# Kernel optimization log

Measured on AMD Instinct MI355X. Metric: run time of the kernel, lower is better.

Reference implementation:

```python
import jax, jax.numpy as jnp
import numpy as np

B, IN, U = 4096, 256, 128
G, LW, LB = 1000, 64, 32


def setup_inputs() -> dict:
    key = jax.random.key(0)
    ks = jax.random.split(key, 9)
    return {
        "x": jax.random.normal(ks[0], (B, IN), dtype=jnp.float32),
        "eps_w": jax.random.normal(ks[1], (B, LW), dtype=jnp.float32),
        "eps_b": jax.random.normal(ks[2], (B, LB), dtype=jnp.float32),
        "zw_mu": jax.random.normal(ks[3], (G, LW), dtype=jnp.float32) * 0.05,
        "zw_sigma": jax.random.normal(ks[4], (G, LW), dtype=jnp.float32),
        "Wf": jax.random.normal(ks[5], (LW, IN * U), dtype=jnp.float32) * (1.0 / np.sqrt(LW)),
        "zb_mu": jnp.zeros((G, LB), dtype=jnp.float32),
        "zb_sigma": jax.random.normal(ks[6], (G, LB), dtype=jnp.float32),
        "Bf": jax.random.normal(ks[7], (LB, U), dtype=jnp.float32) * (1.0 / np.sqrt(LB)),
        "gid": jax.random.randint(ks[8], (B,), 0, G, dtype=jnp.int32),
    }


def reference(x, eps_w, eps_b, zw_mu, zw_sigma, Wf, zb_mu, zb_sigma, Bf, gid):
    # --- multilevel weights: gather group posterior, reparameterized sample ---
    mu_w = zw_mu[gid]                                  # [B, LW]
    sig_w = jax.nn.softplus(zw_sigma[gid])             # [B, LW]
    zw_samp = mu_w + sig_w * eps_w                     # [B, LW]
    w = (zw_samp @ Wf).reshape(B, IN, U)               # factor out to per-example weights
    # --- multilevel bias ---
    mu_b = zb_mu[gid]                                  # [B, LB]
    sig_b = jax.nn.softplus(zb_sigma[gid])             # [B, LB]
    b = (mu_b + sig_b * eps_b) @ Bf                    # [B, U]
    # --- batched per-example matmul: w^T @ x  (tf.matmul(w, x, transpose_a=True)) ---
    out = jnp.einsum("bi,biu->bu", x, w) + b           # [B, U]
    return out  # activation is None (linear)
```

## Files before the change

kernel.cpp:

```cpp
#include <hip/hip_runtime.h>
#include <hip/hip_bf16.h>
#include <stdint.h>

#define B_SZ   4096
#define IN_SZ  256
#define U_SZ   128
#define G_SZ   1000
#define LW_SZ  64
#define LB_SZ  32
#define K_SZ   (LW_SZ * IN_SZ)

#define BM     128
#define BK     64
#define KSPL   16
#define NSTEP  16
#define NTILE  (K_SZ / BK)
#define CHUNK  (BK * U_SZ)

typedef __attribute__((ext_vector_type(8))) short  bf16x8;
typedef __attribute__((ext_vector_type(4))) float  f32x4;
typedef __attribute__((ext_vector_type(8))) _Float16 f16x8;
typedef __attribute__((ext_vector_type(2))) _Float16 f16x2;
typedef __attribute__((ext_vector_type(4))) _Float16 f16x4;

typedef const void __attribute__((address_space(1)))* gas_ptr;
typedef void __attribute__((address_space(3)))* las_ptr;

__device__ __forceinline__ ushort f2bf(float f) {
    unsigned u = __float_as_uint(f);
    u += 0x7fffu + ((u >> 16) & 1u);
    return (ushort)(u >> 16);
}

__device__ __forceinline__ float softplus_f(float v) {
    return fmaxf(v, 0.0f) + log1pf(__expf(-fabsf(v)));
}

__global__ __launch_bounds__(256) void fmd_prep(
    const float* __restrict__ Wf, const float* __restrict__ x,
    short* __restrict__ wfT, short* __restrict__ xh)
{
    const int tid = threadIdx.x;
    if (blockIdx.x < NTILE) {
        const int t = blockIdx.x;
        __shared__ float lds[64 * 133];
        #pragma unroll
        for (int it = 0; it < 8; ++it) {
            int idx = it * 256 + tid;
            int kk = idx >> 5, u4 = idx & 31;
            float4 v = *reinterpret_cast<const float4*>(&Wf[(t * 64 + kk) * U_SZ + u4 * 4]);
            *reinterpret_cast<float4*>(&lds[kk * 133 + u4 * 4]) = v;
        }
        __syncthreads();
        short* chunk = wfT + t * CHUNK;
        #pragma unroll
        for (int g = 0; g < 4; ++g) {
            int p = g * 2048 + tid * 8;
            int u = p >> 6;
            int cc = p & 63;
            int kk0 = cc ^ ((u & 7) << 3);
            union { _Float16 h[8]; f16x8 v; } pk;
            #pragma unroll
            for (int j = 0; j < 8; ++j)
                pk.h[j] = (_Float16)lds[(kk0 + j) * 133 + u];
            *reinterpret_cast<f16x8*>(&chunk[p]) = pk.v;
        }
    } else {
        const int bb = blockIdx.x - NTILE;
        const int mt = bb >> 2, c = bb & 3;
        short* chunk = xh + bb * CHUNK;
        #pragma unroll
        for (int g = 0; g < 4; ++g) {
            int p = g * 2048 + tid * 8;
            int r = p >> 6;
            int cc0 = (p & 63) ^ ((r & 7) << 3);
            const float* src = &x[(mt * BM + r) * IN_SZ + c * 64 + cc0];
            float4 a = *reinterpret_cast<const float4*>(src);
            float4 b = *reinterpret_cast<const float4*>(src + 4);
            union { _Float16 h[8]; f16x8 v; } pk;
            pk.h[0] = (_Float16)a.x; pk.h[1] = (_Float16)a.y;
            pk.h[2] = (_Float16)a.z; pk.h[3] = (_Float16)a.w;
            pk.h[4] = (_Float16)b.x; pk.h[5] = (_Float16)b.y;
            pk.h[6] = (_Float16)b.z; pk.h[7] = (_Float16)b.w;
            *reinterpret_cast<f16x8*>(&chunk[p]) = pk.v;
        }
    }
}

__global__ __launch_bounds__(256, 2) void fmd_gemm5(
    const short* __restrict__ xh,
    const short* __restrict__ wfT,
    const float* __restrict__ zw_mu,
    const float* __restrict__ zw_sigma,
    const float* __restrict__ eps_w,
    const int*   __restrict__ gid,
    _Float16*    __restrict__ part)
{
    const int tid  = threadIdx.x;
    const int lane = tid & 63;
    const int wid  = tid >> 6;
    const int wr   = wid >> 1;
    const int wc   = wid & 1;
    const int bid  = blockIdx.x;
    const int ks   = bid & (KSPL - 1);
    const int mt   = bid >> 4;
    const int m0   = mt * BM;

    __shared__ short As[CHUNK];
    __shared__ short Bs[3][CHUNK];

    f16x2 zwp[4][4];
    #pragma unroll
    for (int m = 0; m < 4; ++m) {
        int row = wr * 64 + m * 16 + (lane & 15);
        int b   = m0 + row;
        int g   = gid[b];
        float4 mu = *reinterpret_cast<const float4*>(&zw_mu[g * LW_SZ + ks * 4]);
        float4 sg = *reinterpret_cast<const float4*>(&zw_sigma[g * LW_SZ + ks * 4]);
        float4 ep = *reinterpret_cast<const float4*>(&eps_w[b * LW_SZ + ks * 4]);
        float v0 = mu.x + softplus_f(sg.x) * ep.x;
        float v1 = mu.y + softplus_f(sg.y) * ep.y;
        float v2 = mu.z + softplus_f(sg.z) * ep.z;
        float v3 = mu.w + softplus_f(sg.w) * ep.w;
        _Float16 h0 = (_Float16)v0, h1 = (_Float16)v1, h2 = (_Float16)v2, h3 = (_Float16)v3;
        zwp[m][0] = (f16x2){h0, h0};
        zwp[m][1] = (f16x2){h1, h1};
        zwp[m][2] = (f16x2){h2, h2};
        zwp[m][3] = (f16x2){h3, h3};
    }

    const int soff = wid * 2048 + lane * 8;
    const int doff = wid * 2048;

    {
        const short* sB0 = wfT + (ks * 16 + 0) * CHUNK;
        const short* sA0 = xh + (mt * 4 + 0) * CHUNK;
        const short* sB1 = wfT + (ks * 16 + 4) * CHUNK;
        #pragma unroll
        for (int j = 0; j < 4; ++j)
            __builtin_amdgcn_global_load_lds((gas_ptr)(sB0 + soff + j * 512),
                                             (las_ptr)(&Bs[0][doff + j * 512]), 16, 0, 0);
        #pragma unroll
        for (int j = 0; j < 4; ++j)
            __builtin_amdgcn_global_load_lds((gas_ptr)(sA0 + soff + j * 512),
                                             (las_ptr)(&As[doff + j * 512]), 16, 0, 0);
        #pragma unroll
        for (int j = 0; j < 4; ++j)
            __builtin_amdgcn_global_load_lds((gas_ptr)(sB1 + soff + j * 512),
                                             (las_ptr)(&Bs[1][doff + j * 512]), 16, 0, 0);
    }
    asm volatile("s_waitcnt vmcnt(4)" ::: "memory");
    __builtin_amdgcn_s_barrier();

    f32x4 acc[4][4];
    #pragma unroll
    for (int m = 0; m < 4; ++m)
        #pragma unroll
        for (int n = 0; n < 4; ++n)
            acc[m][n] = (f32x4){0.f, 0.f, 0.f, 0.f};

    for (int c = 0; c < 4; ++c) {
        union { f16x8 v8; f16x2 v2[4]; } areg[2][4];

        #pragma unroll
        for (int li = 0; li < 4; ++li) {
            const int s = c * 4 + li;

            if (s + 2 < NSTEP) {
                const int s2 = s + 2;
                const short* sB = wfT + (ks * 16 + (s2 & 3) * 4 + (s2 >> 2)) * CHUNK;
                short* dB = &Bs[s2 % 3][doff];
                #pragma unroll
                for (int j = 0; j < 4; ++j)
                    __builtin_amdgcn_global_load_lds((gas_ptr)(sB + soff + j * 512),
                                                     (las_ptr)(dB + j * 512), 16, 0, 0);
            }
            if (li == 1 && c < 3) {
                const short* sA = xh + (mt * 4 + c + 1) * CHUNK;
                #pragma unroll
                for (int j = 0; j < 4; ++j)
                    __builtin_amdgcn_global_load_lds((gas_ptr)(sA + soff + j * 512),
                                                     (las_ptr)(&As[doff + j * 512]), 16, 0, 0);
            }
            __builtin_amdgcn_sched_barrier(0);

            if (li == 0) {
                #pragma unroll
                for (int kb = 0; kb < 2; ++kb)
                    #pragma unroll
                    for (int m = 0; m < 4; ++m) {
                        int row = wr * 64 + m * 16 + (lane & 15);
                        int si = (row * BK + kb * 32 + (lane >> 4) * 8) ^ ((row & 7) << 3);
                        areg[kb][m].v8 = *reinterpret_cast<const f16x8*>(&As[si]);
                    }
            }

            const short* Bb = Bs[s % 3];
            __builtin_amdgcn_s_setprio(1);
            #pragma unroll
            for (int kb = 0; kb < 2; ++kb) {
                union { f16x8 v8; f16x2 v2[4]; } bfv[4], as_[4];
                #pragma unroll
                for (int n = 0; n < 4; ++n) {
                    int rowu = wc * 64 + n * 16 + (lane & 15);
                    int si = (rowu * BK + kb * 32 + (lane >> 4) * 8) ^ ((rowu & 7) << 3);
                    bfv[n].v8 = *reinterpret_cast<const f16x8*>(&Bb[si]);
                }
                #pragma unroll
                for (int m = 0; m < 4; ++m) {
                    #pragma unroll
                    for (int w = 0; w < 4; ++w)
                        as_[m].v2[w] = areg[kb][m].v2[w] * zwp[m][li];
                }
                #pragma unroll
                for (int m = 0; m < 4; ++m)
                    #pragma unroll
                    for (int n = 0; n < 4; ++n)
                        acc[m][n] = __builtin_amdgcn_mfma_f32_16x16x32_f16(
                            as_[m].v8, bfv[n].v8, acc[m][n], 0, 0, 0);
            }
            __builtin_amdgcn_s_setprio(0);

            if (li == 0) {
                asm volatile("s_waitcnt vmcnt(4) lgkmcnt(0)" ::: "memory");
                __builtin_amdgcn_s_barrier();
            } else if (li == 1) {
                if (c < 3) { asm volatile("s_waitcnt vmcnt(8) lgkmcnt(0)" ::: "memory"); }
                else       { asm volatile("s_waitcnt vmcnt(4) lgkmcnt(0)" ::: "memory"); }
                __builtin_amdgcn_s_barrier();
            } else if (li == 2) {
                if (c < 3) { asm volatile("s_waitcnt vmcnt(8) lgkmcnt(0)" ::: "memory"); }
                else       { asm volatile("s_waitcnt vmcnt(0) lgkmcnt(0)" ::: "memory"); }
                __builtin_amdgcn_s_barrier();
            } else {
                if (s != NSTEP - 1) {
                    asm volatile("s_waitcnt vmcnt(4) lgkmcnt(0)" ::: "memory");
                    __builtin_amdgcn_s_barrier();
                }
            }
        }
    }

    _Float16* dst = part + (size_t)ks * (B_SZ * U_SZ);
    #pragma unroll
    for (int m = 0; m < 4; ++m) {
        int row0 = m0 + wr * 64 + m * 16 + ((lane >> 4) << 2);
        #pragma unroll
        for (int n = 0; n < 4; ++n) {
            int col = wc * 64 + n * 16 + (lane & 15);
            #pragma unroll
            for (int j = 0; j < 4; ++j)
                __builtin_nontemporal_store((_Float16)acc[m][n][j],
                                            &dst[(row0 + j) * U_SZ + col]);
        }
    }
}

__global__ __launch_bounds__(256) void fmd_reduce3(
    const _Float16* __restrict__ part,
    const float* __restrict__ eps_b,
    const float* __restrict__ zb_mu,
    const float* __restrict__ zb_sigma,
    const float* __restrict__ Bf,
    const int*   __restrict__ gid,
    float*       __restrict__ out)
{
    const int tid = threadIdx.x;
    const int bid = blockIdx.x;
    const int i8  = bid * 256 + tid;
    const int r   = tid >> 4;
    const int u0  = (tid & 15) * 8;

    __shared__ float zb[16][33];
    {
        int e = tid;
        int rr = e >> 5, cc = e & 31;
        int b2 = bid * 16 + rr;
        int g  = gid[b2];
        zb[rr][cc] = zb_mu[g * LB_SZ + cc]
                   + softplus_f(zb_sigma[g * LB_SZ + cc]) * eps_b[b2 * LB_SZ + cc];
        e += 256; rr = e >> 5; cc = e & 31;
        b2 = bid * 16 + rr;
        g  = gid[b2];
        zb[rr][cc] = zb_mu[g * LB_SZ + cc]
                   + softplus_f(zb_sigma[g * LB_SZ + cc]) * eps_b[b2 * LB_SZ + cc];
    }
    __syncthreads();

    f32x4 a0 = (f32x4){0.f, 0.f, 0.f, 0.f};
    f32x4 a1 = (f32x4){0.f, 0.f, 0.f, 0.f};
    #pragma unroll
    for (int l = 0; l < LB_SZ; ++l) {
        float z = zb[r][l];
        f32x4 b0 = *reinterpret_cast<const f32x4*>(&Bf[l * U_SZ + u0]);
        f32x4 b1 = *reinterpret_cast<const f32x4*>(&Bf[l * U_SZ + u0 + 4]);
        a0 += z * b0;
        a1 += z * b1;
    }

    #pragma unroll
    for (int ks = 0; ks < KSPL; ++ks) {
        f16x8 p = __builtin_nontemporal_load(
            reinterpret_cast<const f16x8*>(&part[(size_t)ks * (B_SZ * U_SZ) + (size_t)i8 * 8]));
        a0[0] += (float)p[0]; a0[1] += (float)p[1];
        a0[2] += (float)p[2]; a0[3] += (float)p[3];
        a1[0] += (float)p[4]; a1[1] += (float)p[5];
        a1[2] += (float)p[6]; a1[3] += (float)p[7];
    }
    *reinterpret_cast<f32x4*>(&out[(size_t)i8 * 8])     = a0;
    *reinterpret_cast<f32x4*>(&out[(size_t)i8 * 8 + 4]) = a1;
}

__global__ __launch_bounds__(256) void fmd_bias(
    const float* __restrict__ eps_b,
    const float* __restrict__ zb_mu,
    const float* __restrict__ zb_sigma,
    const float* __restrict__ Bf,
    const int*   __restrict__ gid,
    float*       __restrict__ out)
{
    const int half = threadIdx.x >> 7;
    const int u    = threadIdx.x & 127;
    const int b    = blockIdx.x * 2 + half;

    __shared__ float zb[2][LB_SZ];
    if (u < LB_SZ) {
        int g = gid[b];
        float sg = softplus_f(zb_sigma[g * LB_SZ + u]);
        zb[half][u] = zb_mu[g * LB_SZ + u] + sg * eps_b[b * LB_SZ + u];
    }
    __syncthreads();

    float acc = 0.0f;
    #pragma unroll
    for (int l = 0; l < LB_SZ; ++l)
        acc += zb[half][l] * Bf[l * U_SZ + u];
    out[b * U_SZ + u] = acc;
}

__global__ __launch_bounds__(256, 2) void fmd_gemm_legacy(
    const float* __restrict__ x,
    const float* __restrict__ eps_w,
    const float* __restrict__ zw_mu,
    const float* __restrict__ zw_sigma,
    const float* __restrict__ Wf,
    const int*   __restrict__ gid,
    float*       __restrict__ out)
{
    const int tid  = threadIdx.x;
    const int lane = tid & 63;
    const int wid  = tid >> 6;
    const int wr   = wid >> 1;
    const int wc   = wid & 1;
    const int bid  = blockIdx.x;
    const int ks   = bid & (KSPL - 1);
    const int mt   = bid >> 4;
    const int m0   = mt * BM;

    __shared__ short As[BM * BK];
    __shared__ short Bs[U_SZ * BK];
    __shared__ float zw_s[BM][4];

    for (int it = tid; it < BM * 4; it += 256) {
        int r = it >> 2, lloc = it & 3;
        int b = m0 + r;
        int g = gid[b];
        int l = ks * 4 + lloc;
        float sg = softplus_f(zw_sigma[g * LW_SZ + l]);
        zw_s[r][lloc] = zw_mu[g * LW_SZ + l] + sg * eps_w[b * LW_SZ + l];
    }

    f32x4 acc[4][4];
    #pragma unroll
    for (int m = 0; m < 4; ++m)
        #pragma unroll
        for (int n = 0; n < 4; ++n)
            acc[m][n] = (f32x4){0.f, 0.f, 0.f, 0.f};

    for (int s = 0; s < NSTEP; ++s) {
        __syncthreads();
        const int li = s >> 2;
        const int i0 = (s & 3) * BK;
        const int k0 = ks * (K_SZ / KSPL) + s * BK;

        #pragma unroll
        for (int it = 0; it < 8; ++it) {
            int idx = it * 256 + tid;
            int r = idx >> 4, c4 = idx & 15;
            float4 xv = *reinterpret_cast<const float4*>(&x[(m0 + r) * IN_SZ + i0 + c4 * 4]);
            float zw = zw_s[r][li];
            ushort h0 = f2bf(xv.x * zw), h1 = f2bf(xv.y * zw);
            ushort h2 = f2bf(xv.z * zw), h3 = f2bf(xv.w * zw);
            unsigned long long pw = (unsigned long long)h0
                                  | ((unsigned long long)h1 << 16)
                                  | ((unsigned long long)h2 << 32)
                                  | ((unsigned long long)h3 << 48);
            int si = (r * BK + c4 * 4) ^ ((r & 7) << 3);
            *reinterpret_cast<unsigned long long*>(&As[si]) = pw;
        }
        #pragma unroll
        for (int it = 0; it < 4; ++it) {
            int idx = it * 256 + tid;
            int u = idx & 127, kg = idx >> 7;
            union { ushort h[8]; bf16x8 v; } pk;
            #pragma unroll
            for (int j = 0; j < 8; ++j)
                pk.h[j] = f2bf(Wf[(k0 + kg * 8 + j) * U_SZ + u]);
            int si = (u * BK + kg * 8) ^ ((u & 7) << 3);
            *reinterpret_cast<bf16x8*>(&Bs[si]) = pk.v;
        }
        __syncthreads();

        #pragma unroll
        for (int kb = 0; kb < 2; ++kb) {
            bf16x8 af[4], bfr[4];
            #pragma unroll
            for (int m = 0; m < 4; ++m) {
                int row = wr * 64 + m * 16 + (lane & 15);
                int si = (row * BK + kb * 32 + (lane >> 4) * 8) ^ ((row & 7) << 3);
                af[m] = *reinterpret_cast<const bf16x8*>(&As[si]);
            }
            #pragma unroll
            for (int n = 0; n < 4; ++n) {
                int rowu = wc * 64 + n * 16 + (lane & 15);
                int si = (rowu * BK + kb * 32 + (lane >> 4) * 8) ^ ((rowu & 7) << 3);
                bfr[n] = *reinterpret_cast<const bf16x8*>(&Bs[si]);
            }
            #pragma unroll
            for (int m = 0; m < 4; ++m)
                #pragma unroll
                for (int n = 0; n < 4; ++n)
                    acc[m][n] = __builtin_amdgcn_mfma_f32_16x16x32_bf16(af[m], bfr[n], acc[m][n], 0, 0, 0);
        }
    }

    #pragma unroll
    for (int m = 0; m < 4; ++m) {
        int row0 = m0 + wr * 64 + m * 16 + ((lane >> 4) << 2);
        #pragma unroll
        for (int n = 0; n < 4; ++n) {
            int col = wc * 64 + n * 16 + (lane & 15);
            #pragma unroll
            for (int j = 0; j < 4; ++j)
                atomicAdd(&out[(row0 + j) * U_SZ + col], acc[m][n][j]);
        }
    }
}

extern "C" void kernel_launch(void* const* d_in, const int* in_sizes, int n_in,
                              void* d_out, int out_size, void* d_ws, size_t ws_size,
                              hipStream_t stream) {
    const float* x        = (const float*)d_in[0];
    const float* eps_w    = (const float*)d_in[1];
    const float* eps_b    = (const float*)d_in[2];
    const float* zw_mu    = (const float*)d_in[3];
    const float* zw_sigma = (const float*)d_in[4];
    const float* Wf       = (const float*)d_in[5];
    const float* zb_mu    = (const float*)d_in[6];
    const float* zb_sigma = (const float*)d_in[7];
    const float* Bf       = (const float*)d_in[8];
    const int*   gid      = (const int*)d_in[9];
    float* out = (float*)d_out;

    const size_t WFT_BYTES  = (size_t)K_SZ * U_SZ * 2;
    const size_t XH_OFF     = WFT_BYTES;
    const size_t XH_BYTES   = (size_t)B_SZ * IN_SZ * 2;
    const size_t PART_OFF   = XH_OFF + XH_BYTES;
    const size_t PART_BYTES = (size_t)KSPL * B_SZ * U_SZ * 2;

    if (ws_size >= PART_OFF + PART_BYTES) {
        short*     wfT  = (short*)d_ws;
        short*     xh   = (short*)((char*)d_ws + XH_OFF);
        _Float16*  part = (_Float16*)((char*)d_ws + PART_OFF);
        fmd_prep<<<NTILE + (B_SZ / BM) * 4, 256, 0, stream>>>(Wf, x, wfT, xh);
        fmd_gemm5<<<(B_SZ / BM) * KSPL, 256, 0, stream>>>(
            xh, wfT, zw_mu, zw_sigma, eps_w, gid, part);
        fmd_reduce3<<<(B_SZ * U_SZ) / 2048, 256, 0, stream>>>(
            part, eps_b, zb_mu, zb_sigma, Bf, gid, out);
    } else {
        fmd_bias<<<B_SZ / 2, 256, 0, stream>>>(eps_b, zb_mu, zb_sigma, Bf, gid, out);
        fmd_gemm_legacy<<<(B_SZ / BM) * KSPL, 256, 0, stream>>>(
            x, eps_w, zw_mu, zw_sigma, Wf, gid, out);
    }
}
```

Measured before the change: 48.84 us.

## Pre-swizzle operands into MFMA fragment order and load directly to registers

```diff
diff --git a/kernel.cpp b/kernel.cpp
--- a/kernel.cpp
+++ b/kernel.cpp
@@ -11,20 +11,15 @@
 #define K_SZ   (LW_SZ * IN_SZ)
 
 #define BM     128
-#define BK     64
 #define KSPL   16
 #define NSTEP  16
-#define NTILE  (K_SZ / BK)
-#define CHUNK  (BK * U_SZ)
+#define NTILE  (K_SZ / 64)
+#define TSH    8192
 
 typedef __attribute__((ext_vector_type(8))) short  bf16x8;
 typedef __attribute__((ext_vector_type(4))) float  f32x4;
 typedef __attribute__((ext_vector_type(8))) _Float16 f16x8;
 typedef __attribute__((ext_vector_type(2))) _Float16 f16x2;
-typedef __attribute__((ext_vector_type(4))) _Float16 f16x4;
-
-typedef const void __attribute__((address_space(1)))* gas_ptr;
-typedef void __attribute__((address_space(3)))* las_ptr;
 
 __device__ __forceinline__ ushort f2bf(float f) {
     unsigned u = __float_as_uint(f);
@@ -34,6 +29,14 @@
 
 __device__ __forceinline__ float softplus_f(float v) {
     return fmaxf(v, 0.0f) + log1pf(__expf(-fabsf(v)));
+}
+
+__device__ __forceinline__ f16x8 mulzw(f16x8 a, f16x2 z) {
+    union { f16x8 v8; f16x2 v2[4]; } in, out;
+    in.v8 = a;
+    #pragma unroll
+    for (int w = 0; w < 4; ++w) out.v2[w] = in.v2[w] * z;
+    return out.v8;
 }
 
 __global__ __launch_bounds__(256) void fmd_prep(
@@ -52,29 +55,36 @@
             *reinterpret_cast<float4*>(&lds[kk * 133 + u4 * 4]) = v;
         }
         __syncthreads();
-        short* chunk = wfT + t * CHUNK;
-        #pragma unroll
-        for (int g = 0; g < 4; ++g) {
-            int p = g * 2048 + tid * 8;
-            int u = p >> 6;
-            int cc = p & 63;
-            int kk0 = cc ^ ((u & 7) << 3);
+        short* tile = wfT + t * TSH;
+        #pragma unroll
+        for (int it = 0; it < 4; ++it) {
+            int p = it * 256 + tid;
+            int kb  = p >> 9;
+            int u16 = (p >> 6) & 7;
+            int l   = p & 63;
+            int u   = u16 * 16 + (l & 15);
+            int kk0 = kb * 32 + (l >> 4) * 8;
             union { _Float16 h[8]; f16x8 v; } pk;
             #pragma unroll
             for (int j = 0; j < 8; ++j)
                 pk.h[j] = (_Float16)lds[(kk0 + j) * 133 + u];
-            *reinterpret_cast<f16x8*>(&chunk[p]) = pk.v;
+            *reinterpret_cast<f16x8*>(&tile[p * 8]) = pk.v;
         }
     } else {
         const int bb = blockIdx.x - NTILE;
         const int mt = bb >> 2, c = bb & 3;
-        short* chunk = xh + bb * CHUNK;
-        #pragma unroll
-        for (int g = 0; g < 4; ++g) {
-            int p = g * 2048 + tid * 8;
-            int r = p >> 6;
-            int cc0 = (p & 63) ^ ((r & 7) << 3);
-            const float* src = &x[(mt * BM + r) * IN_SZ + c * 64 + cc0];
+        short* tile = xh + bb * TSH;
+        #pragma unroll
+        for (int it = 0; it < 4; ++it) {
+            int p = it * 256 + tid;
+            int frag = p >> 6;
+            int l    = p & 63;
+            int wr2  = frag >> 3;
+            int m2   = (frag >> 1) & 3;
+            int kb   = frag & 1;
+            int row  = mt * 128 + wr2 * 64 + m2 * 16 + (l & 15);
+            int col  = c * 64 + kb * 32 + (l >> 4) * 8;
+            const float* src = &x[row * IN_SZ + col];
             float4 a = *reinterpret_cast<const float4*>(src);
             float4 b = *reinterpret_cast<const float4*>(src + 4);
             union { _Float16 h[8]; f16x8 v; } pk;
@@ -82,12 +92,12 @@
             pk.h[2] = (_Float16)a.z; pk.h[3] = (_Float16)a.w;
             pk.h[4] = (_Float16)b.x; pk.h[5] = (_Float16)b.y;
             pk.h[6] = (_Float16)b.z; pk.h[7] = (_Float16)b.w;
-            *reinterpret_cast<f16x8*>(&chunk[p]) = pk.v;
-        }
-    }
-}
-
-__global__ __launch_bounds__(256, 2) void fmd_gemm5(
+            *reinterpret_cast<f16x8*>(&tile[p * 8]) = pk.v;
+        }
+    }
+}
+
+__global__ __launch_bounds__(256, 2) void fmd_gemm6(
     const short* __restrict__ xh,
     const short* __restrict__ wfT,
     const float* __restrict__ zw_mu,
@@ -105,9 +115,7 @@
     const int ks   = bid & (KSPL - 1);
     const int mt   = bid >> 4;
     const int m0   = mt * BM;
-
-    __shared__ short As[CHUNK];
-    __shared__ short Bs[3][CHUNK];
+    const int lane8 = lane * 8;
 
     f16x2 zwp[4][4];
     #pragma unroll
@@ -129,28 +137,26 @@
         zwp[m][3] = (f16x2){h3, h3};
     }
 
-    const int soff = wid * 2048 + lane * 8;
-    const int doff = wid * 2048;
+    f16x8 areg[2][2][4];
+    f16x8 breg[2][2][4];
 
     {
-        const short* sB0 = wfT + (ks * 16 + 0) * CHUNK;
-        const short* sA0 = xh + (mt * 4 + 0) * CHUNK;
-        const short* sB1 = wfT + (ks * 16 + 4) * CHUNK;
-        #pragma unroll
-        for (int j = 0; j < 4; ++j)
-            __builtin_amdgcn_global_load_lds((gas_ptr)(sB0 + soff + j * 512),
-                                             (las_ptr)(&Bs[0][doff + j * 512]), 16, 0, 0);
-        #pragma unroll
-        for (int j = 0; j < 4; ++j)
-            __builtin_amdgcn_global_load_lds((gas_ptr)(sA0 + soff + j * 512),
-                                             (las_ptr)(&As[doff + j * 512]), 16, 0, 0);
-        #pragma unroll
-        for (int j = 0; j < 4; ++j)
-            __builtin_amdgcn_global_load_lds((gas_ptr)(sB1 + soff + j * 512),
-                                             (las_ptr)(&Bs[1][doff + j * 512]), 16, 0, 0);
-    }
-    asm volatile("s_waitcnt vmcnt(4)" ::: "memory");
-    __builtin_amdgcn_s_barrier();
+        const short* ap = xh + (mt * 4 + 0) * TSH;
+        #pragma unroll
+        for (int kb = 0; kb < 2; ++kb)
+            #pragma unroll
+            for (int m = 0; m < 4; ++m)
+                areg[0][kb][m] = *reinterpret_cast<const f16x8*>(
+                    &ap[((wr * 4 + m) * 2 + kb) * 512 + lane8]);
+        const int t0 = (ks * 4 + 0) * 4 + 0;
+        const short* bp = wfT + t0 * TSH;
+        #pragma unroll
+        for (int kb = 0; kb < 2; ++kb)
+            #pragma unroll
+            for (int n = 0; n < 4; ++n)
+                breg[0][kb][n] = *reinterpret_cast<const f16x8*>(
+                    &bp[(kb * 8 + wc * 4 + n) * 512 + lane8]);
+    }
 
     f32x4 acc[4][4];
     #pragma unroll
@@ -159,84 +165,45 @@
         for (int n = 0; n < 4; ++n)
             acc[m][n] = (f32x4){0.f, 0.f, 0.f, 0.f};
 
+    #pragma unroll
     for (int c = 0; c < 4; ++c) {
-        union { f16x8 v8; f16x2 v2[4]; } areg[2][4];
-
         #pragma unroll
         for (int li = 0; li < 4; ++li) {
             const int s = c * 4 + li;
 
-            if (s + 2 < NSTEP) {
-                const int s2 = s + 2;
-                const short* sB = wfT + (ks * 16 + (s2 & 3) * 4 + (s2 >> 2)) * CHUNK;
-                short* dB = &Bs[s2 % 3][doff];
-                #pragma unroll
-                for (int j = 0; j < 4; ++j)
-                    __builtin_amdgcn_global_load_lds((gas_ptr)(sB + soff + j * 512),
-                                                     (las_ptr)(dB + j * 512), 16, 0, 0);
-            }
-            if (li == 1 && c < 3) {
-                const short* sA = xh + (mt * 4 + c + 1) * CHUNK;
-                #pragma unroll
-                for (int j = 0; j < 4; ++j)
-                    __builtin_amdgcn_global_load_lds((gas_ptr)(sA + soff + j * 512),
-                                                     (las_ptr)(&As[doff + j * 512]), 16, 0, 0);
-            }
-            __builtin_amdgcn_sched_barrier(0);
-
-            if (li == 0) {
+            if (s + 1 < NSTEP) {
+                const int sn = s + 1;
+                const int t  = (ks * 4 + (sn & 3)) * 4 + (sn >> 2);
+                const short* bp = wfT + t * TSH;
                 #pragma unroll
                 for (int kb = 0; kb < 2; ++kb)
                     #pragma unroll
-                    for (int m = 0; m < 4; ++m) {
-                        int row = wr * 64 + m * 16 + (lane & 15);
-                        int si = (row * BK + kb * 32 + (lane >> 4) * 8) ^ ((row & 7) << 3);
-                        areg[kb][m].v8 = *reinterpret_cast<const f16x8*>(&As[si]);
-                    }
+                    for (int n = 0; n < 4; ++n)
+                        breg[sn & 1][kb][n] = *reinterpret_cast<const f16x8*>(
+                            &bp[(kb * 8 + wc * 4 + n) * 512 + lane8]);
             }
-
-            const short* Bb = Bs[s % 3];
-            __builtin_amdgcn_s_setprio(1);
+            if (li == 2 && c < 3) {
+                const short* ap = xh + (mt * 4 + c + 1) * TSH;
+                #pragma unroll
+                for (int kb = 0; kb < 2; ++kb)
+                    #pragma unroll
+                    for (int m = 0; m < 4; ++m)
+                        areg[(c + 1) & 1][kb][m] = *reinterpret_cast<const f16x8*>(
+                            &ap[((wr * 4 + m) * 2 + kb) * 512 + lane8]);
+            }
+
             #pragma unroll
             for (int kb = 0; kb < 2; ++kb) {
-                union { f16x8 v8; f16x2 v2[4]; } bfv[4], as_[4];
+                f16x8 as_[4];
                 #pragma unroll
-                for (int n = 0; n < 4; ++n) {
-                    int rowu = wc * 64 + n * 16 + (lane & 15);
-                    int si = (rowu * BK + kb * 32 + (lane >> 4) * 8) ^ ((rowu & 7) << 3);
-                    bfv[n].v8 = *reinterpret_cast<const f16x8*>(&Bb[si]);
-                }
-                #pragma unroll
-                for (int m = 0; m < 4; ++m) {
-                    #pragma unroll
-                    for (int w = 0; w < 4; ++w)
-                        as_[m].v2[w] = areg[kb][m].v2[w] * zwp[m][li];
-                }
+                for (int m = 0; m < 4; ++m)
+                    as_[m] = mulzw(areg[c & 1][kb][m], zwp[m][li]);
                 #pragma unroll
                 for (int m = 0; m < 4; ++m)
                     #pragma unroll
                     for (int n = 0; n < 4; ++n)
                         acc[m][n] = __builtin_amdgcn_mfma_f32_16x16x32_f16(
-                            as_[m].v8, bfv[n].v8, acc[m][n], 0, 0, 0);
-            }
-            __builtin_amdgcn_s_setprio(0);
-
-            if (li == 0) {
-                asm volatile("s_waitcnt vmcnt(4) lgkmcnt(0)" ::: "memory");
-                __builtin_amdgcn_s_barrier();
-            } else if (li == 1) {
-                if (c < 3) { asm volatile("s_waitcnt vmcnt(8) lgkmcnt(0)" ::: "memory"); }
-                else       { asm volatile("s_waitcnt vmcnt(4) lgkmcnt(0)" ::: "memory"); }
-                __builtin_amdgcn_s_barrier();
-            } else if (li == 2) {
-                if (c < 3) { asm volatile("s_waitcnt vmcnt(8) lgkmcnt(0)" ::: "memory"); }
-                else       { asm volatile("s_waitcnt vmcnt(0) lgkmcnt(0)" ::: "memory"); }
-                __builtin_amdgcn_s_barrier();
-            } else {
-                if (s != NSTEP - 1) {
-                    asm volatile("s_waitcnt vmcnt(4) lgkmcnt(0)" ::: "memory");
-                    __builtin_amdgcn_s_barrier();
-                }
+                            as_[m], breg[s & 1][kb][n], acc[m][n], 0, 0, 0);
             }
         }
     }
@@ -250,13 +217,12 @@
             int col = wc * 64 + n * 16 + (lane & 15);
             #pragma unroll
             for (int j = 0; j < 4; ++j)
-                __builtin_nontemporal_store((_Float16)acc[m][n][j],
-                                            &dst[(row0 + j) * U_SZ + col]);
-        }
-    }
-}
-
-__global__ __launch_bounds__(256) void fmd_reduce3(
+                dst[(row0 + j) * U_SZ + col] = (_Float16)acc[m][n][j];
+        }
+    }
+}
+
+__global__ __launch_bounds__(256) void fmd_reduce4(
     const _Float16* __restrict__ part,
     const float* __restrict__ eps_b,
     const float* __restrict__ zb_mu,
@@ -300,8 +266,8 @@
 
     #pragma unroll
     for (int ks = 0; ks < KSPL; ++ks) {
-        f16x8 p = __builtin_nontemporal_load(
-            reinterpret_cast<const f16x8*>(&part[(size_t)ks * (B_SZ * U_SZ) + (size_t)i8 * 8]));
+        f16x8 p = *reinterpret_cast<const f16x8*>(
+            &part[(size_t)ks * (B_SZ * U_SZ) + (size_t)i8 * 8]);
         a0[0] += (float)p[0]; a0[1] += (float)p[1];
         a0[2] += (float)p[2]; a0[3] += (float)p[3];
         a1[0] += (float)p[4]; a1[1] += (float)p[5];
@@ -357,8 +323,8 @@
     const int mt   = bid >> 4;
     const int m0   = mt * BM;
 
-    __shared__ short As[BM * BK];
-    __shared__ short Bs[U_SZ * BK];
+    __shared__ short As[BM * 64];
+    __shared__ short Bs[U_SZ * 64];
     __shared__ float zw_s[BM][4];
 
     for (int it = tid; it < BM * 4; it += 256) {
@@ -380,8 +346,8 @@
     for (int s = 0; s < NSTEP; ++s) {
         __syncthreads();
         const int li = s >> 2;
-        const int i0 = (s & 3) * BK;
-        const int k0 = ks * (K_SZ / KSPL) + s * BK;
+        const int i0 = (s & 3) * 64;
+        const int k0 = ks * (K_SZ / KSPL) + s * 64;
 
         #pragma unroll
         for (int it = 0; it < 8; ++it) {
@@ -395,7 +361,7 @@
                                   | ((unsigned long long)h1 << 16)
                                   | ((unsigned long long)h2 << 32)
                                   | ((unsigned long long)h3 << 48);
-            int si = (r * BK + c4 * 4) ^ ((r & 7) << 3);
+            int si = (r * 64 + c4 * 4) ^ ((r & 7) << 3);
             *reinterpret_cast<unsigned long long*>(&As[si]) = pw;
         }
         #pragma unroll
@@ -406,7 +372,7 @@
             #pragma unroll
             for (int j = 0; j < 8; ++j)
                 pk.h[j] = f2bf(Wf[(k0 + kg * 8 + j) * U_SZ + u]);
-            int si = (u * BK + kg * 8) ^ ((u & 7) << 3);
+            int si = (u * 64 + kg * 8) ^ ((u & 7) << 3);
             *reinterpret_cast<bf16x8*>(&Bs[si]) = pk.v;
         }
         __syncthreads();
@@ -417,13 +383,13 @@
             #pragma unroll
             for (int m = 0; m < 4; ++m) {
                 int row = wr * 64 + m * 16 + (lane & 15);
-                int si = (row * BK + kb * 32 + (lane >> 4) * 8) ^ ((row & 7) << 3);
+                int si = (row * 64 + kb * 32 + (lane >> 4) * 8) ^ ((row & 7) << 3);
                 af[m] = *reinterpret_cast<const bf16x8*>(&As[si]);
             }
             #pragma unroll
             for (int n = 0; n < 4; ++n) {
                 int rowu = wc * 64 + n * 16 + (lane & 15);
-                int si = (rowu * BK + kb * 32 + (lane >> 4) * 8) ^ ((rowu & 7) << 3);
+                int si = (rowu * 64 + kb * 32 + (lane >> 4) * 8) ^ ((rowu & 7) << 3);
                 bfr[n] = *reinterpret_cast<const bf16x8*>(&Bs[si]);
             }
             #pragma unroll
@@ -473,9 +439,9 @@
         short*     xh   = (short*)((char*)d_ws + XH_OFF);
         _Float16*  part = (_Float16*)((char*)d_ws + PART_OFF);
         fmd_prep<<<NTILE + (B_SZ / BM) * 4, 256, 0, stream>>>(Wf, x, wfT, xh);
-        fmd_gemm5<<<(B_SZ / BM) * KSPL, 256, 0, stream>>>(
+        fmd_gemm6<<<(B_SZ / BM) * KSPL, 256, 0, stream>>>(
             xh, wfT, zw_mu, zw_sigma, eps_w, gid, part);
-        fmd_reduce3<<<(B_SZ * U_SZ) / 2048, 256, 0, stream>>>(
+        fmd_reduce4<<<(B_SZ * U_SZ) / 2048, 256, 0, stream>>>(
             part, eps_b, zb_mu, zb_sigma, Bf, gid, out);
     } else {
         fmd_bias<<<B_SZ / 2, 256, 0, stream>>>(eps_b, zb_mu, zb_sigma, Bf, gid, out);
```

Result: faster. 43.81 us (-10.3%).
